# Optimization experiments

Hardware: AMD Instinct MI355X
Metric: run time of the kernel (lower is better)

Reference implementation:

```python
import jax, jax.numpy as jnp
import numpy as np

NUM_BUCKETS = 64
MAX_DISTANCE = 50000.0


def setup_inputs() -> dict:
    R, I, N, E, H = 64, 512, 4, 256, 8
    key = jax.random.key(0)
    ks = jax.random.split(key, 12)
    p = lambda k, shape: (jax.random.normal(k, shape, dtype=jnp.float32) * 0.02)
    return {
        "x": jax.random.normal(ks[0], (R, I, N, E), dtype=jnp.float32),
        "distances": jax.random.randint(ks[1], (N, I, I), 0, 50000).astype(jnp.int32),
        "Wq": p(ks[2], (E, E)), "bq": jnp.zeros((E,), jnp.float32),
        "Wk": p(ks[3], (E, E)), "bk": jnp.zeros((E,), jnp.float32),
        "Wv": p(ks[4], (E, E)), "bv": jnp.zeros((E,), jnp.float32),
        "Wo": p(ks[5], (E, E)), "bo": jnp.zeros((E,), jnp.float32),
        "rel_emb": p(ks[6], (NUM_BUCKETS, H)),
    }


def reference(x, distances, Wq, bq, Wk, bk, Wv, bv, Wo, bo, rel_emb):
    R, I, N, E = x.shape
    H = rel_emb.shape[1]
    D = E // H
    # scaling = head_dim**-0.5 / sqrt(num_rows)
    scaling = (D ** -0.5) / np.sqrt(R)

    def proj(W, b):
        return (jnp.einsum('rine,fe->rinf', x, W) + b).reshape(R, I, N, H, D)

    q = proj(Wq, bq) * scaling
    k = proj(Wk, bk)
    v = proj(Wv, bv)

    # Row-summed attention logits: (H, N, I, J)
    attn_weights = jnp.einsum('rinhd,rjnhd->hnij', q, k)

    # T5-style relative position bias (buckets = linspace boundaries)
    buckets = jnp.linspace(0.0, MAX_DISTANCE, NUM_BUCKETS - 1)
    abs_dist = jnp.abs(distances).astype(jnp.float32)
    # torch.bucketize(right=False) == searchsorted side='left'
    bucket_idx = jnp.searchsorted(buckets, abs_dist, side='left')  # (N, I, J)
    bias = rel_emb[bucket_idx]                  # (N, I, J, H)
    attn_weights = attn_weights + jnp.transpose(bias, (3, 0, 1, 2))

    attn_probs = jax.nn.softmax(attn_weights, axis=-1)  # dropout p=0.0 -> identity

    context = jnp.einsum('hnij,rjnhd->rinhd', attn_probs, v).reshape(R, I, N, E)
    output = jnp.einsum('rine,fe->rinf', context, Wo) + bo
    return output, attn_probs
```

## Files before the change

### kernel.cpp

```cpp
#include <hip/hip_runtime.h>

typedef unsigned short u16;
typedef unsigned int u32;
typedef float f32x4 __attribute__((ext_vector_type(4)));
typedef short bf16x8 __attribute__((ext_vector_type(8)));
typedef unsigned short u16x8 __attribute__((ext_vector_type(8)));

#define SL 33554432u

__device__ __forceinline__ float bf2f(u16 u) {
  u32 v = ((u32)u) << 16;
  return __builtin_bit_cast(float, v);
}
__device__ __forceinline__ u16 f2bf(float f) {
  u32 i = __builtin_bit_cast(u32, f);
  i += 0x7fffu + ((i >> 16) & 1u);
  return (u16)(i >> 16);
}

#define GLDS16(g, l) __builtin_amdgcn_global_load_lds( \
    (const __attribute__((address_space(1))) void*)(g), \
    (__attribute__((address_space(3))) void*)(l), 16, 0, 0)

__device__ __forceinline__ void stage128(const u16* gbase, int ldk, u16* lds, int tid) {
  #pragma unroll
  for (int rep = 0; rep < 4; ++rep) {
    int c = tid + rep * 256;
    int row = c >> 3, slot = c & 7;
    const u16* g = gbase + (size_t)row * ldk + ((slot ^ (row & 7)) << 3);
    GLDS16(g, lds + c * 8);
  }
}

__device__ __forceinline__ void mfma128(const u16* As, const u16* Bs, int lane,
                                        int wm0, int wn0, f32x4 acc[4][4]) {
  #pragma unroll
  for (int kk = 0; kk < 2; ++kk) {
    bf16x8 a[4], b[4];
    #pragma unroll
    for (int mi = 0; mi < 4; ++mi) {
      int r = wm0 + mi * 16 + (lane & 15);
      int c16 = (kk * 4 + (lane >> 4)) ^ (r & 7);
      a[mi] = *(const bf16x8*)(As + r * 64 + c16 * 8);
    }
    #pragma unroll
    for (int ni = 0; ni < 4; ++ni) {
      int r = wn0 + ni * 16 + (lane & 15);
      int c16 = (kk * 4 + (lane >> 4)) ^ (r & 7);
      b[ni] = *(const bf16x8*)(Bs + r * 64 + c16 * 8);
    }
    #pragma unroll
    for (int mi = 0; mi < 4; ++mi)
      #pragma unroll
      for (int ni = 0; ni < 4; ++ni)
        acc[mi][ni] = __builtin_amdgcn_mfma_f32_16x16x32_bf16(a[mi], b[ni], acc[mi][ni], 0, 0, 0);
  }
}

__device__ __forceinline__ void gemm_core(const u16* A, int ldkA, const u16* B, int ldkB,
                                          int NT, u16* As, u16* Bs,
                                          int tid, int lane, int wm0, int wn0,
                                          f32x4 acc[4][4]) {
  for (int t = 0; t < NT; ++t) {
    stage128(A + t * 64, ldkA, As, tid);
    stage128(B + t * 64, ldkB, Bs, tid);
    __syncthreads();
    mfma128(As, Bs, lane, wm0, wn0, acc);
    __syncthreads();
  }
}

__device__ __forceinline__ void stage128_512(const u16* gbase, int ldk, u16* lds, int tid) {
  #pragma unroll
  for (int rep = 0; rep < 2; ++rep) {
    int c = tid + rep * 512;
    int row = c >> 3, slot = c & 7;
    const u16* g = gbase + (size_t)row * ldk + ((slot ^ (row & 7)) << 3);
    GLDS16(g, lds + c * 8);
  }
}

__device__ __forceinline__ void mfma128_8w(const u16* As, const u16* Bs, int lane,
                                           int wm0, int wn0, f32x4 acc[4][2]) {
  #pragma unroll
  for (int kk = 0; kk < 2; ++kk) {
    bf16x8 a[4], b[2];
    #pragma unroll
    for (int mi = 0; mi < 4; ++mi) {
      int r = wm0 + mi * 16 + (lane & 15);
      int c16 = (kk * 4 + (lane >> 4)) ^ (r & 7);
      a[mi] = *(const bf16x8*)(As + r * 64 + c16 * 8);
    }
    #pragma unroll
    for (int ni = 0; ni < 2; ++ni) {
      int r = wn0 + ni * 16 + (lane & 15);
      int c16 = (kk * 4 + (lane >> 4)) ^ (r & 7);
      b[ni] = *(const bf16x8*)(Bs + r * 64 + c16 * 8);
    }
    #pragma unroll
    for (int mi = 0; mi < 4; ++mi)
      #pragma unroll
      for (int ni = 0; ni < 2; ++ni)
        acc[mi][ni] = __builtin_amdgcn_mfma_f32_16x16x32_bf16(a[mi], b[ni], acc[mi][ni], 0, 0, 0);
  }
}

__device__ __forceinline__ void gemm_core_512(const u16* A, int ldkA, const u16* B, int ldkB,
                                              int NT, u16* As, u16* Bs,
                                              int tid, int lane, int wm0, int wn0,
                                              f32x4 acc[4][2]) {
  for (int t = 0; t < NT; ++t) {
    stage128_512(A + t * 64, ldkA, As, tid);
    stage128_512(B + t * 64, ldkB, Bs, tid);
    __syncthreads();
    mfma128_8w(As, Bs, lane, wm0, wn0, acc);
    __syncthreads();
  }
}

__global__ __launch_bounds__(256) void k_castx(const float* __restrict__ src,
                                               u16* __restrict__ dst) {
  int idx = blockIdx.x * 256 + threadIdx.x;
  const float4* s = (const float4*)src;
  float4 a = s[(size_t)idx * 2], b = s[(size_t)idx * 2 + 1];
  u16x8 o;
  o[0] = f2bf(a.x); o[1] = f2bf(a.y); o[2] = f2bf(a.z); o[3] = f2bf(a.w);
  o[4] = f2bf(b.x); o[5] = f2bf(b.y); o[6] = f2bf(b.z); o[7] = f2bf(b.w);
  *(u16x8*)(dst + (size_t)idx * 8) = o;
}

__global__ __launch_bounds__(256) void k_castw(
    const float* __restrict__ Wq, const float* __restrict__ Wk,
    const float* __restrict__ Wv, const float* __restrict__ Wo,
    u16* __restrict__ Wb) {
  int idx = blockIdx.x * 256 + threadIdx.x;
  int w = idx >> 13, off = idx & 8191;
  const float* src = (w == 0) ? Wq : (w == 1) ? Wk : (w == 2) ? Wv : Wo;
  const float4* s = (const float4*)(src + (size_t)off * 8);
  float4 a = s[0], b = s[1];
  u16x8 o;
  o[0] = f2bf(a.x); o[1] = f2bf(a.y); o[2] = f2bf(a.z); o[3] = f2bf(a.w);
  o[4] = f2bf(b.x); o[5] = f2bf(b.y); o[6] = f2bf(b.z); o[7] = f2bf(b.w);
  *(u16x8*)(Wb + (size_t)w * 65536 + (size_t)off * 8) = o;
}

__global__ __launch_bounds__(512) void k_proj_mm(
    const u16* __restrict__ xb, const u16* __restrict__ Wb,
    const float* __restrict__ bq, const float* __restrict__ bk, const float* __restrict__ bv,
    u16* __restrict__ qt, u16* __restrict__ kt, u16* __restrict__ vt, float scaling) {
  __shared__ __align__(16) u16 As[128 * 64];
  __shared__ __align__(16) u16 Bs[128 * 64];
  const int tid = threadIdx.x, lane = tid & 63, wave = tid >> 6;
  const int wm0 = (wave >> 2) * 64, wn0 = (wave & 3) * 32;
  const int m0 = blockIdx.x * 128, n0 = blockIdx.y * 128, w = blockIdx.z;

  f32x4 acc[4][2];
  #pragma unroll
  for (int mi = 0; mi < 4; ++mi)
    #pragma unroll
    for (int ni = 0; ni < 2; ++ni) acc[mi][ni] = (f32x4){0.f, 0.f, 0.f, 0.f};

  gemm_core_512(xb + (size_t)m0 * 256, 256, Wb + w * 65536 + (size_t)n0 * 256, 256,
                4, As, Bs, tid, lane, wm0, wn0, acc);

  const float* bias = (w == 0) ? bq : (w == 1) ? bk : bv;
  u16* dst = (w == 0) ? qt : (w == 1) ? kt : vt;
  const float sc = (w == 0) ? scaling : 1.0f;

  #pragma unroll
  for (int mi = 0; mi < 4; ++mi)
    #pragma unroll
    for (int ni = 0; ni < 2; ++ni) {
      int f = n0 + wn0 + ni * 16 + (lane & 15);
      int h = f >> 5, d = f & 31;
      float bb = bias[f];
      #pragma unroll
      for (int q = 0; q < 4; ++q) {
        int m = m0 + wm0 + mi * 16 + (lane >> 4) * 4 + q;
        int n = m & 3, i = (m >> 2) & 511, r = m >> 11;
        size_t o = ((size_t)((n * 8 + h) * 512 + i)) * 2048 + r * 32 + d;
        dst[o] = f2bf((acc[mi][ni][q] + bb) * sc);
      }
    }
}

__global__ __launch_bounds__(512) void k_attn_mm(
    const u16* __restrict__ qt, const u16* __restrict__ kt, u16* __restrict__ lgt) {
  __shared__ __align__(16) u16 As[128 * 64];
  __shared__ __align__(16) u16 Bs[128 * 64];
  const int tid = threadIdx.x, lane = tid & 63, wave = tid >> 6;
  const int wm0 = (wave >> 2) * 64, wn0 = (wave & 3) * 32;
  const int bid = blockIdx.x;
  const int sb = (bid & 7) * 64 + (bid >> 3);
  const int nh = sb >> 4, tt = sb & 15;
  const int m0 = (tt >> 2) * 128, n0 = (tt & 3) * 128;

  f32x4 acc[4][2];
  #pragma unroll
  for (int mi = 0; mi < 4; ++mi)
    #pragma unroll
    for (int ni = 0; ni < 2; ++ni) acc[mi][ni] = (f32x4){0.f, 0.f, 0.f, 0.f};

  const size_t base = (size_t)nh * 512 * 2048;
  gemm_core_512(qt + base + (size_t)m0 * 2048, 2048, kt + base + (size_t)n0 * 2048, 2048,
                32, As, Bs, tid, lane, wm0, wn0, acc);

  #pragma unroll
  for (int mi = 0; mi < 4; ++mi)
    #pragma unroll
    for (int ni = 0; ni < 2; ++ni) {
      int col = n0 + wn0 + ni * 16 + (lane & 15);
      #pragma unroll
      for (int q = 0; q < 4; ++q) {
        int row = m0 + wm0 + mi * 16 + (lane >> 4) * 4 + q;
        lgt[(size_t)nh * 262144 + (size_t)row * 512 + col] = f2bf(acc[mi][ni][q]);
      }
    }
}

__global__ __launch_bounds__(256) void k_softmax(
    const u16* __restrict__ lgt, const int* __restrict__ dist, const float* __restrict__ rel,
    float* __restrict__ probs, u16* __restrict__ pbf) {
  const int t = threadIdx.x;
  const int lane = t & 63, wv = t >> 6;
  const int b = blockIdx.x;
  const int i = b & 511, n = b >> 9;

  const int* dr = dist + ((size_t)n * 512 + i) * 512 + lane * 8;
  int4 dA = *(const int4*)dr, dB = *(const int4*)(dr + 4);
  int dd[8] = {dA.x, dA.y, dA.z, dA.w, dB.x, dB.y, dB.z, dB.w};
  int u[8];
  #pragma unroll
  for (int j = 0; j < 8; ++j) {
    int v = dd[j] < 0 ? -dd[j] : dd[j];
    int q = (62 * v + 49999) / 50000; if (q > 63) q = 63;
    u[j] = q;
  }

  #pragma unroll
  for (int hh = 0; hh < 2; ++hh) {
    const int h = wv * 2 + hh;
    const int nh = n * 8 + h;
    const u16* lr = lgt + ((size_t)nh * 512 + i) * 512 + lane * 8;
    u16x8 L = *(const u16x8*)lr;
    float vj[8];
    float mx = -1e30f;
    #pragma unroll
    for (int j = 0; j < 8; ++j) {
      vj[j] = bf2f(L[j]) + rel[u[j] * 8 + h];
      mx = fmaxf(mx, vj[j]);
    }
    #pragma unroll
    for (int off = 32; off; off >>= 1) mx = fmaxf(mx, __shfl_xor(mx, off));
    float s = 0.f;
    #pragma unroll
    for (int j = 0; j < 8; ++j) { vj[j] = __expf(vj[j] - mx); s += vj[j]; }
    #pragma unroll
    for (int off = 32; off; off >>= 1) s += __shfl_xor(s, off);
    float inv = 1.0f / s;
    float4 pa, pb;
    pa.x = vj[0]*inv; pa.y = vj[1]*inv; pa.z = vj[2]*inv; pa.w = vj[3]*inv;
    pb.x = vj[4]*inv; pb.y = vj[5]*inv; pb.z = vj[6]*inv; pb.w = vj[7]*inv;
    size_t po = ((size_t)(h * 4 + n) * 512 + i) * 512 + lane * 8;
    *(float4*)(probs + po) = pa;
    *(float4*)(probs + po + 4) = pb;
    u16x8 pc;
    pc[0]=f2bf(pa.x); pc[1]=f2bf(pa.y); pc[2]=f2bf(pa.z); pc[3]=f2bf(pa.w);
    pc[4]=f2bf(pb.x); pc[5]=f2bf(pb.y); pc[6]=f2bf(pb.z); pc[7]=f2bf(pb.w);
    size_t pq = ((size_t)nh * 512 + i) * 512 + lane * 8;
    *(u16x8*)(pbf + pq) = pc;
  }
}

__global__ __launch_bounds__(256) void k_vtrans(const u16* __restrict__ vt, u16* __restrict__ vtt) {
  __shared__ u16 ts[64][72];
  const int b = blockIdx.x;
  const int ct_ = b & 31, it = (b >> 5) & 7, nh = b >> 8;
  const int i0 = it * 64, c0 = ct_ * 64;
  const int t = threadIdx.x;
  #pragma unroll
  for (int rep = 0; rep < 2; ++rep) {
    int c = t + rep * 256;
    int r = c >> 3, q = c & 7;
    u16x8 v = *(const u16x8*)(vt + ((size_t)nh * 512 + i0 + r) * 2048 + c0 + q * 8);
    #pragma unroll
    for (int j = 0; j < 8; ++j) ts[r][q * 8 + j] = v[j];
  }
  __syncthreads();
  #pragma unroll
  for (int rep = 0; rep < 2; ++rep) {
    int c = t + rep * 256;
    int rr = c >> 3, q = c & 7;
    u16x8 o;
    #pragma unroll
    for (int j = 0; j < 8; ++j) o[j] = ts[q * 8 + j][rr];
    *(u16x8*)(vtt + ((size_t)nh * 2048 + c0 + rr) * 512 + i0 + q * 8) = o;
  }
}

__global__ __launch_bounds__(256) void k_ctx_mm(
    const u16* __restrict__ vtt, const u16* __restrict__ pbf, u16* __restrict__ ct) {
  __shared__ __align__(16) u16 lds[16640];
  u16* As = lds;
  u16* Bs = lds + 8192;
  u16* ts = lds;
  const int tid = threadIdx.x, lane = tid & 63, wave = tid >> 6;
  const int wm0 = (wave >> 1) * 64, wn0 = (wave & 1) * 64;
  const int bid = blockIdx.x;
  const int sb = (bid & 7) * 256 + (bid >> 3);
  const int nh = sb >> 6, tt = sb & 63;
  const int m0 = (tt >> 2) * 128, n0 = (tt & 3) * 128;
  const int n = nh >> 3, h = nh & 7;

  f32x4 acc[4][4];
  #pragma unroll
  for (int mi = 0; mi < 4; ++mi)
    #pragma unroll
    for (int ni = 0; ni < 4; ++ni) acc[mi][ni] = (f32x4){0.f, 0.f, 0.f, 0.f};

  gemm_core(vtt + (size_t)nh * 1048576 + (size_t)m0 * 512, 512,
            pbf + (size_t)nh * 262144 + (size_t)n0 * 512, 512,
            8, As, Bs, tid, lane, wm0, wn0, acc);

  #pragma unroll
  for (int mi = 0; mi < 4; ++mi)
    #pragma unroll
    for (int ni = 0; ni < 4; ++ni) {
      int i_l = wn0 + ni * 16 + (lane & 15);
      #pragma unroll
      for (int q = 0; q < 4; ++q) {
        int c_l = wm0 + mi * 16 + (lane >> 4) * 4 + q;
        ts[i_l * 130 + c_l] = f2bf(acc[mi][ni][q]);
      }
    }
  __syncthreads();
  #pragma unroll
  for (int cc = 0; cc < 2; ++cc) {
    int ch = tid + cc * 256;
    int i_l = ch & 127, r_l = ch >> 7;
    const u16* src = ts + i_l * 130 + r_l * 32;
    int rr = (m0 >> 5) + r_l;
    size_t o = ((size_t)((rr * 512 + n0 + i_l) * 4 + n)) * 256 + h * 32;
    #pragma unroll
    for (int j = 0; j < 4; ++j)
      *(u16x8*)(ct + o + j * 8) = *(const u16x8*)(src + j * 8);
  }
}

__global__ __launch_bounds__(256) void k_oproj_mm(
    const u16* __restrict__ ct, const u16* __restrict__ Wob,
    const float* __restrict__ bo, float* __restrict__ out) {
  __shared__ __align__(16) u16 As[128 * 64];
  __shared__ __align__(16) u16 Bs[128 * 64];
  const int tid = threadIdx.x, lane = tid & 63, wave = tid >> 6;
  const int wm0 = (wave >> 1) * 64, wn0 = (wave & 1) * 64;
  const int bid = blockIdx.x;
  const int sb = (bid & 7) * 256 + (bid >> 3);
  const int m0 = (sb >> 1) * 128, n0 = (sb & 1) * 128;

  f32x4 acc[4][4];
  #pragma unroll
  for (int mi = 0; mi < 4; ++mi)
    #pragma unroll
    for (int ni = 0; ni < 4; ++ni) acc[mi][ni] = (f32x4){0.f, 0.f, 0.f, 0.f};

  gemm_core(ct + (size_t)m0 * 256, 256, Wob + (size_t)n0 * 256, 256,
            4, As, Bs, tid, lane, wm0, wn0, acc);

  #pragma unroll
  for (int mi = 0; mi < 4; ++mi)
    #pragma unroll
    for (int ni = 0; ni < 4; ++ni) {
      int col = n0 + wn0 + ni * 16 + (lane & 15);
      float bb = bo[col];
      #pragma unroll
      for (int q = 0; q < 4; ++q) {
        int row = m0 + wm0 + mi * 16 + (lane >> 4) * 4 + q;
        out[(size_t)row * 256 + col] = acc[mi][ni][q] + bb;
      }
    }
}

extern "C" void kernel_launch(void* const* d_in, const int* in_sizes, int n_in,
                              void* d_out, int out_size, void* d_ws, size_t ws_size,
                              hipStream_t stream) {
  const float* x  = (const float*)d_in[0];
  const int* dist = (const int*)d_in[1];
  const float* Wq = (const float*)d_in[2];
  const float* bq = (const float*)d_in[3];
  const float* Wk = (const float*)d_in[4];
  const float* bk = (const float*)d_in[5];
  const float* Wv = (const float*)d_in[6];
  const float* bv = (const float*)d_in[7];
  const float* Wo = (const float*)d_in[8];
  const float* bo = (const float*)d_in[9];
  const float* rel = (const float*)d_in[10];
  float* out = (float*)d_out;
  float* probs = out + (size_t)SL;

  u16* ws = (u16*)d_ws;
  u16* xb  = ws;
  u16* qt  = ws + (size_t)SL;
  u16* kt  = ws + (size_t)2 * SL;
  u16* vt  = ws + (size_t)3 * SL;
  u16* lgt = xb;
  u16* pbf = qt;
  u16* vtt = kt;
  u16* ctb = xb;
  u16* Wb  = ws + (size_t)4 * SL;

  const float scaling = 0.022097086912079608f;

  k_castx  <<<16384, 256, 0, stream>>>(x, xb);
  k_castw  <<<128, 256, 0, stream>>>(Wq, Wk, Wv, Wo, Wb);
  k_proj_mm<<<dim3(1024, 2, 3), 512, 0, stream>>>(xb, Wb, bq, bk, bv, qt, kt, vt, scaling);
  k_attn_mm<<<512, 512, 0, stream>>>(qt, kt, lgt);
  k_softmax<<<2048, 256, 0, stream>>>(lgt, dist, rel, probs, pbf);
  k_vtrans <<<8192, 256, 0, stream>>>(vt, vtt);
  k_ctx_mm <<<2048, 256, 0, stream>>>(vtt, pbf, ctb);
  k_oproj_mm<<<2048, 256, 0, stream>>>(ctb, Wb + 196608, bo, out);
}
```

Before: 358.6 us.

## Fuse QKV projection A-tile reuse and double-buffer attention logits GEMM

```diff
diff --git a/kernel.cpp b/kernel.cpp
--- a/kernel.cpp
+++ b/kernel.cpp
@@ -102,19 +102,6 @@
       #pragma unroll
       for (int ni = 0; ni < 2; ++ni)
         acc[mi][ni] = __builtin_amdgcn_mfma_f32_16x16x32_bf16(a[mi], b[ni], acc[mi][ni], 0, 0, 0);
-  }
-}
-
-__device__ __forceinline__ void gemm_core_512(const u16* A, int ldkA, const u16* B, int ldkB,
-                                              int NT, u16* As, u16* Bs,
-                                              int tid, int lane, int wm0, int wn0,
-                                              f32x4 acc[4][2]) {
-  for (int t = 0; t < NT; ++t) {
-    stage128_512(A + t * 64, ldkA, As, tid);
-    stage128_512(B + t * 64, ldkB, Bs, tid);
-    __syncthreads();
-    mfma128_8w(As, Bs, lane, wm0, wn0, acc);
-    __syncthreads();
   }
 }
 
@@ -148,46 +135,86 @@
     const u16* __restrict__ xb, const u16* __restrict__ Wb,
     const float* __restrict__ bq, const float* __restrict__ bk, const float* __restrict__ bv,
     u16* __restrict__ qt, u16* __restrict__ kt, u16* __restrict__ vt, float scaling) {
-  __shared__ __align__(16) u16 As[128 * 64];
-  __shared__ __align__(16) u16 Bs[128 * 64];
+  __shared__ __align__(16) u16 As[8192];
+  __shared__ __align__(16) u16 Bs[12288];
   const int tid = threadIdx.x, lane = tid & 63, wave = tid >> 6;
-  const int wm0 = (wave >> 2) * 64, wn0 = (wave & 3) * 32;
-  const int m0 = blockIdx.x * 128, n0 = blockIdx.y * 128, w = blockIdx.z;
-
-  f32x4 acc[4][2];
-  #pragma unroll
-  for (int mi = 0; mi < 4; ++mi)
-    #pragma unroll
-    for (int ni = 0; ni < 2; ++ni) acc[mi][ni] = (f32x4){0.f, 0.f, 0.f, 0.f};
-
-  gemm_core_512(xb + (size_t)m0 * 256, 256, Wb + w * 65536 + (size_t)n0 * 256, 256,
-                4, As, Bs, tid, lane, wm0, wn0, acc);
-
-  const float* bias = (w == 0) ? bq : (w == 1) ? bk : bv;
-  u16* dst = (w == 0) ? qt : (w == 1) ? kt : vt;
-  const float sc = (w == 0) ? scaling : 1.0f;
-
-  #pragma unroll
-  for (int mi = 0; mi < 4; ++mi)
-    #pragma unroll
-    for (int ni = 0; ni < 2; ++ni) {
-      int f = n0 + wn0 + ni * 16 + (lane & 15);
-      int h = f >> 5, d = f & 31;
-      float bb = bias[f];
+  const int wm0 = (wave >> 2) * 64, wn0 = (wave & 3) * 16;
+  const int bid = blockIdx.x;
+  const int sb = (bid & 7) * 512 + (bid >> 3);
+  const int mt = sb >> 2, nq = sb & 3;
+  const int m0 = mt * 128, n0 = nq * 64;
+
+  f32x4 acc[3][4];
+  #pragma unroll
+  for (int w = 0; w < 3; ++w)
+    #pragma unroll
+    for (int mi = 0; mi < 4; ++mi) acc[w][mi] = (f32x4){0.f, 0.f, 0.f, 0.f};
+
+  for (int t = 0; t < 4; ++t) {
+    #pragma unroll
+    for (int rep = 0; rep < 2; ++rep) {
+      int c = tid + rep * 512;
+      int row = c >> 3, slot = c & 7;
+      GLDS16(xb + (size_t)(m0 + row) * 256 + t * 64 + ((slot ^ (row & 7)) << 3),
+             As + c * 8);
+    }
+    #pragma unroll
+    for (int rep = 0; rep < 3; ++rep) {
+      int cc = tid + rep * 512;
+      int w = cc >> 9, idx = cc & 511;
+      int row = idx >> 3, slot = idx & 7;
+      GLDS16(Wb + w * 65536 + (size_t)(n0 + row) * 256 + t * 64 + ((slot ^ (row & 7)) << 3),
+             Bs + w * 4096 + idx * 8);
+    }
+    __syncthreads();
+
+    #pragma unroll
+    for (int kk = 0; kk < 2; ++kk) {
+      bf16x8 a[4];
+      #pragma unroll
+      for (int mi = 0; mi < 4; ++mi) {
+        int r = wm0 + mi * 16 + (lane & 15);
+        int c16 = (kk * 4 + (lane >> 4)) ^ (r & 7);
+        a[mi] = *(const bf16x8*)(As + r * 64 + c16 * 8);
+      }
+      int rb = wn0 + (lane & 15);
+      int c16b = (kk * 4 + (lane >> 4)) ^ (rb & 7);
+      #pragma unroll
+      for (int w = 0; w < 3; ++w) {
+        bf16x8 b = *(const bf16x8*)(Bs + w * 4096 + rb * 64 + c16b * 8);
+        #pragma unroll
+        for (int mi = 0; mi < 4; ++mi)
+          acc[w][mi] = __builtin_amdgcn_mfma_f32_16x16x32_bf16(a[mi], b, acc[w][mi], 0, 0, 0);
+      }
+    }
+    __syncthreads();
+  }
+
+  #pragma unroll
+  for (int w = 0; w < 3; ++w) {
+    const float* bias = (w == 0) ? bq : (w == 1) ? bk : bv;
+    u16* dst = (w == 0) ? qt : (w == 1) ? kt : vt;
+    const float sc = (w == 0) ? scaling : 1.0f;
+    int f = n0 + wn0 + (lane & 15);
+    int h = f >> 5, d = f & 31;
+    float bb = bias[f];
+    #pragma unroll
+    for (int mi = 0; mi < 4; ++mi) {
       #pragma unroll
       for (int q = 0; q < 4; ++q) {
         int m = m0 + wm0 + mi * 16 + (lane >> 4) * 4 + q;
         int n = m & 3, i = (m >> 2) & 511, r = m >> 11;
         size_t o = ((size_t)((n * 8 + h) * 512 + i)) * 2048 + r * 32 + d;
-        dst[o] = f2bf((acc[mi][ni][q] + bb) * sc);
-      }
-    }
+        dst[o] = f2bf((acc[w][mi][q] + bb) * sc);
+      }
+    }
+  }
 }
 
 __global__ __launch_bounds__(512) void k_attn_mm(
     const u16* __restrict__ qt, const u16* __restrict__ kt, u16* __restrict__ lgt) {
-  __shared__ __align__(16) u16 As[128 * 64];
-  __shared__ __align__(16) u16 Bs[128 * 64];
+  __shared__ __align__(16) u16 As[2][8192];
+  __shared__ __align__(16) u16 Bs[2][8192];
   const int tid = threadIdx.x, lane = tid & 63, wave = tid >> 6;
   const int wm0 = (wave >> 2) * 64, wn0 = (wave & 3) * 32;
   const int bid = blockIdx.x;
@@ -202,8 +229,21 @@
     for (int ni = 0; ni < 2; ++ni) acc[mi][ni] = (f32x4){0.f, 0.f, 0.f, 0.f};
 
   const size_t base = (size_t)nh * 512 * 2048;
-  gemm_core_512(qt + base + (size_t)m0 * 2048, 2048, kt + base + (size_t)n0 * 2048, 2048,
-                32, As, Bs, tid, lane, wm0, wn0, acc);
+  const u16* A = qt + base + (size_t)m0 * 2048;
+  const u16* B = kt + base + (size_t)n0 * 2048;
+
+  stage128_512(A, 2048, As[0], tid);
+  stage128_512(B, 2048, Bs[0], tid);
+  __syncthreads();
+  for (int t = 0; t < 32; ++t) {
+    int cur = t & 1;
+    if (t + 1 < 32) {
+      stage128_512(A + (t + 1) * 64, 2048, As[cur ^ 1], tid);
+      stage128_512(B + (t + 1) * 64, 2048, Bs[cur ^ 1], tid);
+    }
+    mfma128_8w(As[cur], Bs[cur], lane, wm0, wn0, acc);
+    __syncthreads();
+  }
 
   #pragma unroll
   for (int mi = 0; mi < 4; ++mi)
@@ -413,7 +453,7 @@
 
   k_castx  <<<16384, 256, 0, stream>>>(x, xb);
   k_castw  <<<128, 256, 0, stream>>>(Wq, Wk, Wv, Wo, Wb);
-  k_proj_mm<<<dim3(1024, 2, 3), 512, 0, stream>>>(xb, Wb, bq, bk, bv, qt, kt, vt, scaling);
+  k_proj_mm<<<4096, 512, 0, stream>>>(xb, Wb, bq, bk, bv, qt, kt, vt, scaling);
   k_attn_mm<<<512, 512, 0, stream>>>(qt, kt, lgt);
   k_softmax<<<2048, 256, 0, stream>>>(lgt, dist, rel, probs, pbf);
   k_vtrans <<<8192, 256, 0, stream>>>(vt, vtt);
```

Result: faster. 330.3 us (-7.9%).

## Double-buffer LDS tiles in projection and attention GEMMs

Applied to the files above, without the earlier changes.

```diff
diff --git a/kernel.cpp b/kernel.cpp
--- a/kernel.cpp
+++ b/kernel.cpp
@@ -102,19 +102,6 @@
       #pragma unroll
       for (int ni = 0; ni < 2; ++ni)
         acc[mi][ni] = __builtin_amdgcn_mfma_f32_16x16x32_bf16(a[mi], b[ni], acc[mi][ni], 0, 0, 0);
-  }
-}
-
-__device__ __forceinline__ void gemm_core_512(const u16* A, int ldkA, const u16* B, int ldkB,
-                                              int NT, u16* As, u16* Bs,
-                                              int tid, int lane, int wm0, int wn0,
-                                              f32x4 acc[4][2]) {
-  for (int t = 0; t < NT; ++t) {
-    stage128_512(A + t * 64, ldkA, As, tid);
-    stage128_512(B + t * 64, ldkB, Bs, tid);
-    __syncthreads();
-    mfma128_8w(As, Bs, lane, wm0, wn0, acc);
-    __syncthreads();
   }
 }
 
@@ -148,8 +135,8 @@
     const u16* __restrict__ xb, const u16* __restrict__ Wb,
     const float* __restrict__ bq, const float* __restrict__ bk, const float* __restrict__ bv,
     u16* __restrict__ qt, u16* __restrict__ kt, u16* __restrict__ vt, float scaling) {
-  __shared__ __align__(16) u16 As[128 * 64];
-  __shared__ __align__(16) u16 Bs[128 * 64];
+  __shared__ __align__(16) u16 As[2][8192];
+  __shared__ __align__(16) u16 Bs[2][8192];
   const int tid = threadIdx.x, lane = tid & 63, wave = tid >> 6;
   const int wm0 = (wave >> 2) * 64, wn0 = (wave & 3) * 32;
   const int m0 = blockIdx.x * 128, n0 = blockIdx.y * 128, w = blockIdx.z;
@@ -160,8 +147,21 @@
     #pragma unroll
     for (int ni = 0; ni < 2; ++ni) acc[mi][ni] = (f32x4){0.f, 0.f, 0.f, 0.f};
 
-  gemm_core_512(xb + (size_t)m0 * 256, 256, Wb + w * 65536 + (size_t)n0 * 256, 256,
-                4, As, Bs, tid, lane, wm0, wn0, acc);
+  const u16* A = xb + (size_t)m0 * 256;
+  const u16* B = Wb + w * 65536 + (size_t)n0 * 256;
+
+  stage128_512(A, 256, As[0], tid);
+  stage128_512(B, 256, Bs[0], tid);
+  __syncthreads();
+  for (int t = 0; t < 4; ++t) {
+    int cur = t & 1;
+    if (t + 1 < 4) {
+      stage128_512(A + (t + 1) * 64, 256, As[cur ^ 1], tid);
+      stage128_512(B + (t + 1) * 64, 256, Bs[cur ^ 1], tid);
+    }
+    mfma128_8w(As[cur], Bs[cur], lane, wm0, wn0, acc);
+    __syncthreads();
+  }
 
   const float* bias = (w == 0) ? bq : (w == 1) ? bk : bv;
   u16* dst = (w == 0) ? qt : (w == 1) ? kt : vt;
@@ -186,8 +186,8 @@
 
 __global__ __launch_bounds__(512) void k_attn_mm(
     const u16* __restrict__ qt, const u16* __restrict__ kt, u16* __restrict__ lgt) {
-  __shared__ __align__(16) u16 As[128 * 64];
-  __shared__ __align__(16) u16 Bs[128 * 64];
+  __shared__ __align__(16) u16 As[2][8192];
+  __shared__ __align__(16) u16 Bs[2][8192];
   const int tid = threadIdx.x, lane = tid & 63, wave = tid >> 6;
   const int wm0 = (wave >> 2) * 64, wn0 = (wave & 3) * 32;
   const int bid = blockIdx.x;
@@ -202,8 +202,21 @@
     for (int ni = 0; ni < 2; ++ni) acc[mi][ni] = (f32x4){0.f, 0.f, 0.f, 0.f};
 
   const size_t base = (size_t)nh * 512 * 2048;
-  gemm_core_512(qt + base + (size_t)m0 * 2048, 2048, kt + base + (size_t)n0 * 2048, 2048,
-                32, As, Bs, tid, lane, wm0, wn0, acc);
+  const u16* A = qt + base + (size_t)m0 * 2048;
+  const u16* B = kt + base + (size_t)n0 * 2048;
+
+  stage128_512(A, 2048, As[0], tid);
+  stage128_512(B, 2048, Bs[0], tid);
+  __syncthreads();
+  for (int t = 0; t < 32; ++t) {
+    int cur = t & 1;
+    if (t + 1 < 32) {
+      stage128_512(A + (t + 1) * 64, 2048, As[cur ^ 1], tid);
+      stage128_512(B + (t + 1) * 64, 2048, Bs[cur ^ 1], tid);
+    }
+    mfma128_8w(As[cur], Bs[cur], lane, wm0, wn0, acc);
+    __syncthreads();
+  }
 
   #pragma unroll
   for (int mi = 0; mi < 4; ++mi)
```

After: 362.4 us. About the same (+1.0%).
